# Optimization experiments

Hardware: AMD Instinct MI355X
Metric: run time of the kernel (lower is better)

## Reference

```python
import jax, jax.numpy as jnp
import numpy as np

D = 1024      # query_dim
H = 16        # heads
DH = 64       # dim_head
I = H * DH    # inner_dim = 1024
DC = 768      # context_dim
FF = 4 * D    # ff inner dim = 4096
EPS = 1e-5
SCALE = DH ** -0.5


def setup_inputs() -> dict:
    key = jax.random.key(0)
    ks = jax.random.split(key, 20)
    s = 0.02
    inp = {
        'x': jax.random.normal(ks[0], (2, 2048, D), jnp.float32),
        'context': jax.random.normal(ks[1], (2, 77, DC), jnp.float32),
        'ln1_g': jnp.ones((D,), jnp.float32), 'ln1_b': jnp.zeros((D,), jnp.float32),
        'ln2_g': jnp.ones((D,), jnp.float32), 'ln2_b': jnp.zeros((D,), jnp.float32),
        'ln3_g': jnp.ones((D,), jnp.float32), 'ln3_b': jnp.zeros((D,), jnp.float32),
        'Wq1': jax.random.normal(ks[2], (D, I), jnp.float32) * s,
        'Wk1': jax.random.normal(ks[3], (D, I), jnp.float32) * s,
        'Wv1': jax.random.normal(ks[4], (D, I), jnp.float32) * s,
        'Wo1': jax.random.normal(ks[5], (I, D), jnp.float32) * s,
        'bo1': jnp.zeros((D,), jnp.float32),
        'Wq2': jax.random.normal(ks[6], (D, I), jnp.float32) * s,
        'Wk2': jax.random.normal(ks[7], (DC, I), jnp.float32) * s,
        'Wv2': jax.random.normal(ks[8], (DC, I), jnp.float32) * s,
        'Wo2': jax.random.normal(ks[9], (I, D), jnp.float32) * s,
        'bo2': jnp.zeros((D,), jnp.float32),
        'Wff1': jax.random.normal(ks[10], (D, 2 * FF), jnp.float32) * s,
        'bff1': jnp.zeros((2 * FF,), jnp.float32),
        'Wff2': jax.random.normal(ks[11], (FF, D), jnp.float32) * s,
        'bff2': jnp.zeros((D,), jnp.float32),
    }
    return inp


def layer_norm(x, g, b):
    m = jnp.mean(x, axis=-1, keepdims=True)
    v = jnp.mean(jnp.square(x - m), axis=-1, keepdims=True)
    return (x - m) * jax.lax.rsqrt(v + EPS) * g + b


def cross_attention(x, ctx, Wq, Wk, Wv, Wo, bo):
    # x: [B,N,D], ctx: [B,M,Dc]
    B, N, _ = x.shape
    M = ctx.shape[1]
    q = (x @ Wq).reshape(B, N, H, DH).transpose(0, 2, 1, 3)    # [B,H,N,DH]
    k = (ctx @ Wk).reshape(B, M, H, DH).transpose(0, 2, 1, 3)  # [B,H,M,DH]
    v = (ctx @ Wv).reshape(B, M, H, DH).transpose(0, 2, 1, 3)
    sim = jnp.einsum('bhid,bhjd->bhij', q, k) * SCALE           # [B,H,N,M]
    attn = jax.nn.softmax(sim, axis=-1)
    out = jnp.einsum('bhij,bhjd->bhid', attn, v)                # [B,H,N,DH]
    out = out.transpose(0, 2, 1, 3).reshape(B, N, I)
    return out @ Wo + bo


def reference(x, context, ln1_g, ln1_b, ln2_g, ln2_b, ln3_g, ln3_b,
              Wq1, Wk1, Wv1, Wo1, bo1, Wq2, Wk2, Wv2, Wo2, bo2,
              Wff1, bff1, Wff2, bff2):
    # self-attention
    x = cross_attention(layer_norm(x, ln1_g, ln1_b), layer_norm(x, ln1_g, ln1_b),
                        Wq1, Wk1, Wv1, Wo1, bo1) + x
    # cross-attention
    x = cross_attention(layer_norm(x, ln2_g, ln2_b), context,
                        Wq2, Wk2, Wv2, Wo2, bo2) + x
    # GEGLU feed-forward
    hg = layer_norm(x, ln3_g, ln3_b) @ Wff1 + bff1
    h, gate = hg[..., :FF], hg[..., FF:]
    ff = (h * jax.nn.gelu(gate, approximate=False)) @ Wff2 + bff2
    return ff + x
```

## Files before the change

### kernel.cpp

```cpp
#include <hip/hip_runtime.h>
#include <hip/hip_bf16.h>
#include <math.h>

typedef short short8 __attribute__((ext_vector_type(8)));
typedef float floatx4 __attribute__((ext_vector_type(4)));
typedef unsigned short u16;

#define D_MODEL 1024
#define NH 16
#define DH 64
#define FF_DIM 4096

__device__ __forceinline__ u16 f2b(float f) {
  union { float f; unsigned u; } v; v.f = f;
  unsigned r = (v.u + 0x7fffu + ((v.u >> 16) & 1u)) >> 16;
  return (u16)r;
}
__device__ __forceinline__ u16 f2b_fast(float f) {
  union { float f; unsigned u; } v; v.f = f;
  return (u16)((v.u + 0x8000u) >> 16);
}
__device__ __forceinline__ float b2f(u16 h) {
  union { unsigned u; float f; } v; v.u = ((unsigned)h) << 16;
  return v.f;
}

__device__ __forceinline__ void gl_lds16(const u16* g, u16* l) {
  __builtin_amdgcn_global_load_lds(
      (const __attribute__((address_space(1))) unsigned int*)g,
      (__attribute__((address_space(3))) unsigned int*)l, 16, 0, 0);
}

__launch_bounds__(256)
__global__ void transpose_to_bf16(const float* __restrict__ in, u16* __restrict__ out,
                                  int K, int N, float scale) {
  __shared__ float tile[32][33];
  const int n0 = blockIdx.x * 32;
  const int k0 = blockIdx.y * 32;
  const int tx = threadIdx.x & 31;
  const int ty = threadIdx.x >> 5;
#pragma unroll
  for (int i = 0; i < 4; i++) {
    int k = k0 + ty + i * 8;
    tile[ty + i * 8][tx] = in[(size_t)k * N + (n0 + tx)] * scale;
  }
  __syncthreads();
#pragma unroll
  for (int i = 0; i < 4; i++) {
    int n = n0 + ty + i * 8;
    out[(size_t)n * K + (k0 + tx)] = f2b(tile[tx][ty + i * 8]);
  }
}

struct TransArgs {
  const float* src[6];
  u16* dst[6];
  float scale[6];
};

__launch_bounds__(256)
__global__ void transpose_to_bf16_multi(TransArgs a, int K, int N) {
  __shared__ float tile[32][33];
  const int z = blockIdx.z;
  const float* __restrict__ in = a.src[z];
  u16* __restrict__ out = a.dst[z];
  const float scale = a.scale[z];
  const int n0 = blockIdx.x * 32;
  const int k0 = blockIdx.y * 32;
  const int tx = threadIdx.x & 31;
  const int ty = threadIdx.x >> 5;
#pragma unroll
  for (int i = 0; i < 4; i++) {
    int k = k0 + ty + i * 8;
    tile[ty + i * 8][tx] = in[(size_t)k * N + (n0 + tx)] * scale;
  }
  __syncthreads();
#pragma unroll
  for (int i = 0; i < 4; i++) {
    int n = n0 + ty + i * 8;
    out[(size_t)n * K + (k0 + tx)] = f2b(tile[tx][ty + i * 8]);
  }
}

__launch_bounds__(256)
__global__ void convert_bf16(const float* __restrict__ in, u16* __restrict__ out, int n) {
  int i = blockIdx.x * 256 + threadIdx.x;
  if (i < n) out[i] = f2b(in[i]);
}

__launch_bounds__(256)
__global__ void ln_to_bf16(const float* __restrict__ x, const float* __restrict__ g,
                           const float* __restrict__ b, u16* __restrict__ out) {
  const int row = blockIdx.x;
  const int tid = threadIdx.x;
  const float4 v = ((const float4*)(x + (size_t)row * D_MODEL))[tid];
  float s = v.x + v.y + v.z + v.w;
  float ss = v.x * v.x + v.y * v.y + v.z * v.z + v.w * v.w;
#pragma unroll
  for (int o = 32; o; o >>= 1) { s += __shfl_xor(s, o); ss += __shfl_xor(ss, o); }
  __shared__ float red[8];
  const int wave = tid >> 6, lane = tid & 63;
  if (lane == 0) { red[wave] = s; red[4 + wave] = ss; }
  __syncthreads();
  const float st = red[0] + red[1] + red[2] + red[3];
  const float sst = red[4] + red[5] + red[6] + red[7];
  const float mean = st * (1.0f / D_MODEL);
  const float var = sst * (1.0f / D_MODEL) - mean * mean;
  const float rs = rsqrtf(var + 1e-5f);
  const float4 gv = ((const float4*)g)[tid];
  const float4 bv = ((const float4*)b)[tid];
  ushort4 o4;
  o4.x = f2b((v.x - mean) * rs * gv.x + bv.x);
  o4.y = f2b((v.y - mean) * rs * gv.y + bv.y);
  o4.z = f2b((v.z - mean) * rs * gv.z + bv.z);
  o4.w = f2b((v.w - mean) * rs * gv.w + bv.w);
  ((ushort4*)(out + (size_t)row * D_MODEL))[tid] = o4;
}

template <int EPI>
__launch_bounds__(256)
__global__ void gemm128(const u16* __restrict__ A, const u16* __restrict__ BT,
                        const float* __restrict__ bias, const float* __restrict__ resid,
                        float* __restrict__ Cf, u16* __restrict__ Cb, u16* __restrict__ VT,
                        int K, int lda, int ldb, int ldc) {
  __shared__ __attribute__((aligned(16))) u16 Al[128 * 64];
  __shared__ __attribute__((aligned(16))) u16 Bl[128 * 64];
  const int tid = threadIdx.x, wave = tid >> 6, lane = tid & 63;
  const int lm = lane & 15, lq = lane >> 4;
  const int wr = (wave >> 1) * 64, wc = (wave & 1) * 64;
  const int m0 = blockIdx.y * 128, n0 = blockIdx.x * 128;
  const int x8 = lm & 7;

  floatx4 acc[4][4] = {};

  for (int k0 = 0; k0 < K; k0 += 64) {
#pragma unroll
    for (int it = 0; it < 4; it++) {
      const int c = wave * 256 + it * 64 + lane;
      const int r = c >> 3, s = c & 7;
      const int lc = s ^ (r & 7);
      gl_lds16(A + (size_t)(m0 + r) * lda + k0 + lc * 8, &Al[c * 8]);
      gl_lds16(BT + (size_t)(n0 + r) * ldb + k0 + lc * 8, &Bl[c * 8]);
    }
    __syncthreads();
#pragma unroll
    for (int ks = 0; ks < 2; ks++) {
      short8 af[4], bf[4];
#pragma unroll
      for (int r = 0; r < 4; r++)
        af[r] = *(const short8*)(&Al[(wr + r * 16 + lm) * 64 + ((ks * 4 + lq) ^ x8) * 8]);
#pragma unroll
      for (int c = 0; c < 4; c++)
        bf[c] = *(const short8*)(&Bl[(wc + c * 16 + lm) * 64 + ((ks * 4 + lq) ^ x8) * 8]);
#pragma unroll
      for (int r = 0; r < 4; r++)
#pragma unroll
        for (int c = 0; c < 4; c++)
          acc[r][c] = __builtin_amdgcn_mfma_f32_16x16x32_bf16(af[r], bf[c], acc[r][c], 0, 0, 0);
    }
    __syncthreads();
  }

#pragma unroll
  for (int r = 0; r < 4; r++)
#pragma unroll
    for (int c = 0; c < 4; c++) {
      const int col = n0 + wc + c * 16 + lm;
      const int row0 = m0 + wr + r * 16 + lq * 4;
      if (EPI == 0) {
#pragma unroll
        for (int i = 0; i < 4; i++)
          Cb[(size_t)(row0 + i) * ldc + col] = f2b(acc[r][c][i]);
      } else if (EPI == 1) {
#pragma unroll
        for (int i = 0; i < 4; i++)
          Cf[(size_t)(row0 + i) * ldc + col] =
              acc[r][c][i] + bias[col] + resid[(size_t)(row0 + i) * ldc + col];
      } else {
        if (col < 2048) {
#pragma unroll
          for (int i = 0; i < 4; i++)
            Cb[(size_t)(row0 + i) * ldc + col] = f2b(acc[r][c][i]);
        } else {
          const int d = col - 2048;
          ushort4 pk;
          pk.x = f2b(acc[r][c][0]); pk.y = f2b(acc[r][c][1]);
          pk.z = f2b(acc[r][c][2]); pk.w = f2b(acc[r][c][3]);
          *(ushort4*)(&VT[((size_t)((row0 >> 11) * 1024 + d)) * 2048 + (row0 & 2047)]) = pk;
        }
      }
    }
}

template <int EPI>
__launch_bounds__(256)
__global__ void gemm_n64(const u16* __restrict__ A, const u16* __restrict__ BT,
                         const float* __restrict__ bias, const float* __restrict__ resid,
                         float* __restrict__ Cf, u16* __restrict__ Cb,
                         int K, int lda, int ldb, int ldc) {
  __shared__ __attribute__((aligned(16))) u16 Al[128 * 64];
  __shared__ __attribute__((aligned(16))) u16 Bl[64 * 64];
  const int tid = threadIdx.x, wave = tid >> 6, lane = tid & 63;
  const int lm = lane & 15, lq = lane >> 4;
  const int wr = (wave >> 1) * 64, wc = (wave & 1) * 32;
  const int m0 = blockIdx.y * 128, n0 = blockIdx.x * 64;
  const int x8 = lm & 7;

  floatx4 acc[4][2] = {};

  for (int k0 = 0; k0 < K; k0 += 64) {
#pragma unroll
    for (int it = 0; it < 4; it++) {
      const int c = wave * 256 + it * 64 + lane;
      const int r = c >> 3, s = c & 7;
      const int lc = s ^ (r & 7);
      gl_lds16(A + (size_t)(m0 + r) * lda + k0 + lc * 8, &Al[c * 8]);
    }
#pragma unroll
    for (int it = 0; it < 2; it++) {
      const int c = wave * 128 + it * 64 + lane;
      const int r = c >> 3, s = c & 7;
      const int lc = s ^ (r & 7);
      gl_lds16(BT + (size_t)(n0 + r) * ldb + k0 + lc * 8, &Bl[c * 8]);
    }
    __syncthreads();
#pragma unroll
    for (int ks = 0; ks < 2; ks++) {
      short8 af[4], bf[2];
#pragma unroll
      for (int r = 0; r < 4; r++)
        af[r] = *(const short8*)(&Al[(wr + r * 16 + lm) * 64 + ((ks * 4 + lq) ^ x8) * 8]);
#pragma unroll
      for (int c = 0; c < 2; c++)
        bf[c] = *(const short8*)(&Bl[(wc + c * 16 + lm) * 64 + ((ks * 4 + lq) ^ x8) * 8]);
#pragma unroll
      for (int r = 0; r < 4; r++)
#pragma unroll
        for (int c = 0; c < 2; c++)
          acc[r][c] = __builtin_amdgcn_mfma_f32_16x16x32_bf16(af[r], bf[c], acc[r][c], 0, 0, 0);
    }
    __syncthreads();
  }

#pragma unroll
  for (int r = 0; r < 4; r++)
#pragma unroll
    for (int c = 0; c < 2; c++) {
      const int col = n0 + wc + c * 16 + lm;
      const int row0 = m0 + wr + r * 16 + lq * 4;
      if (EPI == 0) {
#pragma unroll
        for (int i = 0; i < 4; i++)
          Cb[(size_t)(row0 + i) * ldc + col] = f2b(acc[r][c][i]);
      } else {
#pragma unroll
        for (int i = 0; i < 4; i++)
          Cf[(size_t)(row0 + i) * ldc + col] =
              acc[r][c][i] + bias[col] + resid[(size_t)(row0 + i) * ldc + col];
      }
    }
}

__launch_bounds__(256)
__global__ void gemm_geglu(const u16* __restrict__ A, const u16* __restrict__ BT,
                           const float* __restrict__ bias, u16* __restrict__ Cb,
                           int K, int lda, int ldb) {
  __shared__ __attribute__((aligned(16))) u16 Al[128 * 64];
  __shared__ __attribute__((aligned(16))) u16 Bl[64 * 64];
  __shared__ __attribute__((aligned(16))) u16 Bg[64 * 64];
  const int tid = threadIdx.x, wave = tid >> 6, lane = tid & 63;
  const int lm = lane & 15, lq = lane >> 4;
  const int wr = (wave >> 1) * 64, wc = (wave & 1) * 32;
  const int m0 = blockIdx.y * 128, n0 = blockIdx.x * 64;
  const int x8 = lm & 7;

  floatx4 acc[4][2] = {};
  floatx4 accg[4][2] = {};

  for (int k0 = 0; k0 < K; k0 += 64) {
#pragma unroll
    for (int it = 0; it < 4; it++) {
      const int c = wave * 256 + it * 64 + lane;
      const int r = c >> 3, s = c & 7;
      const int lc = s ^ (r & 7);
      gl_lds16(A + (size_t)(m0 + r) * lda + k0 + lc * 8, &Al[c * 8]);
    }
#pragma unroll
    for (int it = 0; it < 2; it++) {
      const int c = wave * 128 + it * 64 + lane;
      const int r = c >> 3, s = c & 7;
      const int lc = s ^ (r & 7);
      gl_lds16(BT + (size_t)(n0 + r) * ldb + k0 + lc * 8, &Bl[c * 8]);
      gl_lds16(BT + (size_t)(n0 + r + FF_DIM) * ldb + k0 + lc * 8, &Bg[c * 8]);
    }
    __syncthreads();
#pragma unroll
    for (int ks = 0; ks < 2; ks++) {
      short8 af[4], bf[2], bg[2];
#pragma unroll
      for (int r = 0; r < 4; r++)
        af[r] = *(const short8*)(&Al[(wr + r * 16 + lm) * 64 + ((ks * 4 + lq) ^ x8) * 8]);
#pragma unroll
      for (int c = 0; c < 2; c++) {
        bf[c] = *(const short8*)(&Bl[(wc + c * 16 + lm) * 64 + ((ks * 4 + lq) ^ x8) * 8]);
        bg[c] = *(const short8*)(&Bg[(wc + c * 16 + lm) * 64 + ((ks * 4 + lq) ^ x8) * 8]);
      }
#pragma unroll
      for (int r = 0; r < 4; r++)
#pragma unroll
        for (int c = 0; c < 2; c++) {
          acc[r][c] = __builtin_amdgcn_mfma_f32_16x16x32_bf16(af[r], bf[c], acc[r][c], 0, 0, 0);
          accg[r][c] = __builtin_amdgcn_mfma_f32_16x16x32_bf16(af[r], bg[c], accg[r][c], 0, 0, 0);
        }
    }
    __syncthreads();
  }

#pragma unroll
  for (int r = 0; r < 4; r++)
#pragma unroll
    for (int c = 0; c < 2; c++) {
      const int col = n0 + wc + c * 16 + lm;
#pragma unroll
      for (int i = 0; i < 4; i++) {
        const int row = m0 + wr + r * 16 + lq * 4 + i;
        const float h = acc[r][c][i] + bias[col];
        const float gt = accg[r][c][i] + bias[col + FF_DIM];
        const float gl = 0.5f * gt * (1.0f + erff(gt * 0.70710678118f));
        Cb[(size_t)row * FF_DIM + col] = f2b(h * gl);
      }
    }
}

#define BM 64
#define BN 64
#define LSTR 40

template <int TRANS>
__launch_bounds__(256)
__global__ void gemm_bt64(const u16* __restrict__ A, const u16* __restrict__ BT,
                          u16* __restrict__ Cb,
                          int M, int N, int K, int lda, int ldb, int ldc, int rowsPerB) {
  __shared__ __attribute__((aligned(16))) u16 Al[BM * LSTR];
  __shared__ __attribute__((aligned(16))) u16 Bl[BN * LSTR];
  const int tid = threadIdx.x, wave = tid >> 6, lane = tid & 63;
  const int wm = (wave >> 1) * 32, wn = (wave & 1) * 32;
  const int lm = lane & 15, lq = lane >> 4;
  const int m0 = blockIdx.y * BM, n0 = blockIdx.x * BN;

  floatx4 acc[2][2] = {};
  const int srow = tid >> 2;
  const int scol = (tid & 3) * 8;
  const bool a_ok = (m0 + srow) < M;

  for (int k0 = 0; k0 < K; k0 += 32) {
    int4 av = make_int4(0, 0, 0, 0);
    if (a_ok) av = *(const int4*)(A + (size_t)(m0 + srow) * lda + k0 + scol);
    *(int4*)(&Al[srow * LSTR + scol]) = av;
    int4 bv = *(const int4*)(BT + (size_t)(n0 + srow) * ldb + k0 + scol);
    *(int4*)(&Bl[srow * LSTR + scol]) = bv;
    __syncthreads();
    short8 af[2], bfr[2];
#pragma unroll
    for (int r = 0; r < 2; r++) af[r] = *(const short8*)(&Al[(wm + r * 16 + lm) * LSTR + lq * 8]);
#pragma unroll
    for (int c = 0; c < 2; c++) bfr[c] = *(const short8*)(&Bl[(wn + c * 16 + lm) * LSTR + lq * 8]);
#pragma unroll
    for (int r = 0; r < 2; r++)
#pragma unroll
      for (int c = 0; c < 2; c++)
        acc[r][c] = __builtin_amdgcn_mfma_f32_16x16x32_bf16(af[r], bfr[c], acc[r][c], 0, 0, 0);
    __syncthreads();
  }

#pragma unroll
  for (int r = 0; r < 2; r++)
#pragma unroll
    for (int c = 0; c < 2; c++) {
      const int col = n0 + wn + c * 16 + lm;
#pragma unroll
      for (int i = 0; i < 4; i++) {
        const int row = m0 + wm + r * 16 + lq * 4 + i;
        if (row < M) {
          if (TRANS == 0) {
            Cb[(size_t)row * ldc + col] = f2b(acc[r][c][i]);
          } else {
            const int bb = row / rowsPerB;
            const int n = row - bb * rowsPerB;
            Cb[((size_t)(bb * 1024 + col)) * 128 + n] = f2b(acc[r][c][i]);
          }
        }
      }
    }
}

__launch_bounds__(512)
__global__ void attn_mfma(const u16* __restrict__ Qg, const u16* __restrict__ Kg,
                          const u16* __restrict__ VTg, u16* __restrict__ Ob,
                          int N, int Mk, int kRowsPerBatch, int ldq, int ldk, int vtld) {
  const int ntiles = N / 128;
  const int bh = blockIdx.x / ntiles;
  const int qt = blockIdx.x % ntiles;
  const int b = bh / NH, h = bh % NH;
  const int tid = threadIdx.x, wave = tid >> 6, lane = tid & 63;
  const int lm = lane & 15, lq = lane >> 4;

  __shared__ __attribute__((aligned(16))) u16 Qs[128 * 64];
  __shared__ __attribute__((aligned(16))) u16 Ks[64 * 64];
  __shared__ __attribute__((aligned(16))) u16 Vt[64 * 64];
  __shared__ __attribute__((aligned(16))) u16 Ps[8][16 * 72];

  const u16* Qh = Qg + (size_t)b * N * ldq + h * DH;
  const u16* Kh = Kg + (size_t)b * kRowsPerBatch * ldk + h * DH;
  const u16* Vh = VTg + (size_t)(b * 1024 + h * DH) * vtld;

  {
    const u16* qsrc = Qh + (size_t)qt * 128 * ldq;
#pragma unroll
    for (int it = 0; it < 2; it++) {
      const int c = wave * 128 + it * 64 + lane;
      const int r = c >> 3, p = c & 7, lc = p ^ (r & 7);
      gl_lds16(qsrc + (size_t)r * ldq + lc * 8, &Qs[c * 8]);
    }
  }
  __syncthreads();
  short8 qf[2];
  qf[0] = *(const short8*)(&Qs[(wave * 16 + lm) * 64 + ((lq) ^ (lm & 7)) * 8]);
  qf[1] = *(const short8*)(&Qs[(wave * 16 + lm) * 64 + ((4 + lq) ^ (lm & 7)) * 8]);

  float lpart[4] = {0.f, 0.f, 0.f, 0.f};
  floatx4 o[4] = {};

  for (int kt = 0; kt < Mk; kt += 64) {
    __syncthreads();
    {
      const u16* ksrc = Kh + (size_t)kt * ldk;
      const u16* vsrc = Vh + kt;
      const int c = wave * 64 + lane;
      const int r = c >> 3, p = c & 7, lc = p ^ (r & 7);
      gl_lds16(ksrc + (size_t)r * ldk + lc * 8, &Ks[c * 8]);
      gl_lds16(vsrc + (size_t)r * vtld + lc * 8, &Vt[c * 8]);
    }
    __syncthreads();

    floatx4 s[4];
#pragma unroll
    for (int ct = 0; ct < 4; ct++) {
      short8 kf0 = *(const short8*)(&Ks[(ct * 16 + lm) * 64 + ((lq) ^ (lm & 7)) * 8]);
      short8 kf1 = *(const short8*)(&Ks[(ct * 16 + lm) * 64 + ((4 + lq) ^ (lm & 7)) * 8]);
      floatx4 z = {};
      z = __builtin_amdgcn_mfma_f32_16x16x32_bf16(qf[0], kf0, z, 0, 0, 0);
      z = __builtin_amdgcn_mfma_f32_16x16x32_bf16(qf[1], kf1, z, 0, 0, 0);
      s[ct] = z;
    }

    if (kt + 64 <= Mk) {
#pragma unroll
      for (int reg = 0; reg < 4; reg++) {
        float p0 = __expf(s[0][reg] - 16.0f);
        float p1 = __expf(s[1][reg] - 16.0f);
        float p2 = __expf(s[2][reg] - 16.0f);
        float p3 = __expf(s[3][reg] - 16.0f);
        lpart[reg] += (p0 + p1) + (p2 + p3);
        const int prow = (lq * 4 + reg) * 72;
        Ps[wave][prow + lm] = f2b_fast(p0);
        Ps[wave][prow + 16 + lm] = f2b_fast(p1);
        Ps[wave][prow + 32 + lm] = f2b_fast(p2);
        Ps[wave][prow + 48 + lm] = f2b_fast(p3);
      }
    } else {
#pragma unroll
      for (int reg = 0; reg < 4; reg++) {
        const int prow = (lq * 4 + reg) * 72;
        float psum = 0.f;
#pragma unroll
        for (int ct = 0; ct < 4; ct++) {
          const bool valid = (kt + ct * 16 + lm) < Mk;
          float p = valid ? __expf(s[ct][reg] - 16.0f) : 0.f;
          psum += p;
          Ps[wave][prow + ct * 16 + lm] = f2b_fast(p);
        }
        lpart[reg] += psum;
      }
    }

    const short8 pf0 = *(const short8*)(&Ps[wave][lm * 72 + lq * 8]);
    const short8 pf1 = *(const short8*)(&Ps[wave][lm * 72 + 32 + lq * 8]);
#pragma unroll
    for (int ct = 0; ct < 4; ct++) {
      short8 vf0 = *(const short8*)(&Vt[(ct * 16 + lm) * 64 + ((lq) ^ (lm & 7)) * 8]);
      short8 vf1 = *(const short8*)(&Vt[(ct * 16 + lm) * 64 + ((4 + lq) ^ (lm & 7)) * 8]);
      o[ct] = __builtin_amdgcn_mfma_f32_16x16x32_bf16(pf0, vf0, o[ct], 0, 0, 0);
      o[ct] = __builtin_amdgcn_mfma_f32_16x16x32_bf16(pf1, vf1, o[ct], 0, 0, 0);
    }
  }

  float inv[4];
#pragma unroll
  for (int reg = 0; reg < 4; reg++) {
    float l = lpart[reg];
    l += __shfl_xor(l, 1); l += __shfl_xor(l, 2);
    l += __shfl_xor(l, 4); l += __shfl_xor(l, 8);
    inv[reg] = 1.0f / l;
  }
#pragma unroll
  for (int ct = 0; ct < 4; ct++)
#pragma unroll
    for (int reg = 0; reg < 4; reg++) {
      const int grow = qt * 128 + wave * 16 + lq * 4 + reg;
      Ob[((size_t)(b * N + grow)) * D_MODEL + h * DH + ct * 16 + lm] =
          f2b(o[ct][reg] * inv[reg]);
    }
}

extern "C" void kernel_launch(void* const* d_in, const int* in_sizes, int n_in,
                              void* d_out, int out_size, void* d_ws, size_t ws_size,
                              hipStream_t stream) {
  const float* x    = (const float*)d_in[0];
  const float* ctx  = (const float*)d_in[1];
  const float* ln1g = (const float*)d_in[2];
  const float* ln1b = (const float*)d_in[3];
  const float* ln2g = (const float*)d_in[4];
  const float* ln2b = (const float*)d_in[5];
  const float* ln3g = (const float*)d_in[6];
  const float* ln3b = (const float*)d_in[7];
  const float* Wq1  = (const float*)d_in[8];
  const float* Wk1  = (const float*)d_in[9];
  const float* Wv1  = (const float*)d_in[10];
  const float* Wo1  = (const float*)d_in[11];
  const float* bo1  = (const float*)d_in[12];
  const float* Wq2  = (const float*)d_in[13];
  const float* Wk2  = (const float*)d_in[14];
  const float* Wv2  = (const float*)d_in[15];
  const float* Wo2  = (const float*)d_in[16];
  const float* bo2  = (const float*)d_in[17];
  const float* Wff1 = (const float*)d_in[18];
  const float* bff1 = (const float*)d_in[19];
  const float* Wff2 = (const float*)d_in[20];
  const float* bff2 = (const float*)d_in[21];
  float* out = (float*)d_out;

  char* ws = (char*)d_ws;
  size_t off = 0;
  auto alloc = [&](size_t bytes) -> char* {
    char* p = ws + off;
    off += (bytes + 255) & ~(size_t)255;
    return p;
  };
  u16* wqkv1T = (u16*)alloc((size_t)3072 * 1024 * 2);
  u16* wo1T   = (u16*)alloc((size_t)1024 * 1024 * 2);
  u16* wq2T   = (u16*)alloc((size_t)1024 * 1024 * 2);
  u16* wk2T   = (u16*)alloc((size_t)1024 * 768 * 2);
  u16* wv2T   = (u16*)alloc((size_t)1024 * 768 * 2);
  u16* wo2T   = (u16*)alloc((size_t)1024 * 1024 * 2);
  u16* wff1T  = (u16*)alloc((size_t)8192 * 1024 * 2);
  u16* wff2T  = (u16*)alloc((size_t)1024 * 4096 * 2);
  u16* xln    = (u16*)alloc((size_t)4096 * 1024 * 2);
  u16* ctxb   = (u16*)alloc((size_t)154 * 768 * 2);
  u16* QKVb   = (u16*)alloc((size_t)4096 * 3072 * 2);
  u16* VTb    = (u16*)alloc((size_t)2048 * 2048 * 2);
  u16* K2b    = (u16*)alloc((size_t)256 * 1024 * 2);
  u16* VT2b   = (u16*)alloc((size_t)2048 * 128 * 2);
  u16* Ob     = (u16*)alloc((size_t)4096 * 1024 * 2);
  float* x1   = (float*)alloc((size_t)4096 * 1024 * 4);
  float* x2   = (float*)alloc((size_t)4096 * 1024 * 4);
  u16* ffin   = (u16*)alloc((size_t)4096 * 4096 * 2);
  u16* Q2b    = ffin;

  dim3 blk(256);
  dim3 blk512(512);

  {
    TransArgs t6;
    t6.src[0] = Wq1;  t6.dst[0] = wqkv1T;                          t6.scale[0] = 1.0f;
    t6.src[1] = Wk1;  t6.dst[1] = wqkv1T + (size_t)1024 * 1024;    t6.scale[1] = 0.125f;
    t6.src[2] = Wv1;  t6.dst[2] = wqkv1T + (size_t)2048 * 1024;    t6.scale[2] = 1.0f;
    t6.src[3] = Wo1;  t6.dst[3] = wo1T;                            t6.scale[3] = 1.0f;
    t6.src[4] = Wq2;  t6.dst[4] = wq2T;                            t6.scale[4] = 1.0f;
    t6.src[5] = Wo2;  t6.dst[5] = wo2T;                            t6.scale[5] = 1.0f;
    transpose_to_bf16_multi<<<dim3(32, 32, 6), blk, 0, stream>>>(t6, 1024, 1024);
  }
  {
    TransArgs t2;
    t2.src[0] = Wk2;  t2.dst[0] = wk2T;  t2.scale[0] = 0.125f;
    t2.src[1] = Wv2;  t2.dst[1] = wv2T;  t2.scale[1] = 1.0f;
    t2.src[2] = Wk2;  t2.dst[2] = wk2T;  t2.scale[2] = 0.125f;
    t2.src[3] = Wk2;  t2.dst[3] = wk2T;  t2.scale[3] = 0.125f;
    t2.src[4] = Wk2;  t2.dst[4] = wk2T;  t2.scale[4] = 0.125f;
    t2.src[5] = Wk2;  t2.dst[5] = wk2T;  t2.scale[5] = 0.125f;
    transpose_to_bf16_multi<<<dim3(32, 24, 2), blk, 0, stream>>>(t2, 768, 1024);
  }
  transpose_to_bf16<<<dim3(256, 32), blk, 0, stream>>>(Wff1, wff1T, 1024, 8192, 1.0f);
  transpose_to_bf16<<<dim3(32, 128), blk, 0, stream>>>(Wff2, wff2T, 4096, 1024, 1.0f);
  convert_bf16<<<(154 * 768 + 255) / 256, blk, 0, stream>>>(ctx, ctxb, 154 * 768);

  ln_to_bf16<<<4096, blk, 0, stream>>>(x, ln1g, ln1b, xln);
  gemm128<2><<<dim3(24, 32), blk, 0, stream>>>(xln, wqkv1T, nullptr, nullptr, nullptr, QKVb,
                                               VTb, 1024, 1024, 1024, 3072);
  attn_mfma<<<2 * NH * (2048 / 128), blk512, 0, stream>>>(QKVb, QKVb + 1024, VTb, Ob,
                                                          2048, 2048, 2048, 3072, 3072, 2048);
  gemm_n64<1><<<dim3(16, 32), blk, 0, stream>>>(Ob, wo1T, bo1, x, x1, nullptr,
                                                1024, 1024, 1024, 1024);

  ln_to_bf16<<<4096, blk, 0, stream>>>(x1, ln2g, ln2b, xln);
  gemm_n64<0><<<dim3(16, 32), blk, 0, stream>>>(xln, wq2T, nullptr, nullptr, nullptr, Q2b,
                                                1024, 1024, 1024, 1024);
  gemm_bt64<0><<<dim3(16, 3), blk, 0, stream>>>(ctxb, wk2T, K2b, 154, 1024, 768, 768, 768, 1024, 77);
  gemm_bt64<1><<<dim3(16, 3), blk, 0, stream>>>(ctxb, wv2T, VT2b, 154, 1024, 768, 768, 768, 1024, 77);
  attn_mfma<<<2 * NH * (2048 / 128), blk512, 0, stream>>>(Q2b, K2b, VT2b, Ob,
                                                          2048, 77, 77, 1024, 1024, 128);
  gemm_n64<1><<<dim3(16, 32), blk, 0, stream>>>(Ob, wo2T, bo2, x1, x2, nullptr,
                                                1024, 1024, 1024, 1024);

  ln_to_bf16<<<4096, blk, 0, stream>>>(x2, ln3g, ln3b, xln);
  gemm_geglu<<<dim3(64, 32), blk, 0, stream>>>(xln, wff1T, bff1, ffin, 1024, 1024, 1024);
  gemm_n64<1><<<dim3(16, 32), blk, 0, stream>>>(ffin, wff2T, bff2, x2, out, nullptr,
                                                4096, 4096, 4096, 1024);
}
```

Measured before the change: 511.1 us.

## Merge weight transposes into one launch and double-buffer GEGLU GEMM

All ten weight transpose-to-bf16 conversions now run in a single kernel launch that uses a flat block index and a per-tensor start table, replacing four separate launches. The GEGLU GEMM gains double-buffered LDS staging, so the next K-tile's global-to-LDS loads are issued before computing on the current tile, hiding load latency. LDS use doubles to roughly 64KB per block, which may lower occupancy. The per-block tensor lookup adds a few scalar instructions per block.

```diff
diff --git a/kernel.cpp b/kernel.cpp
--- a/kernel.cpp
+++ b/kernel.cpp
@@ -31,42 +31,31 @@
       (__attribute__((address_space(3))) unsigned int*)l, 16, 0, 0);
 }
 
+struct PrepArgs {
+  const float* src[10];
+  u16* dst[10];
+  float scale[10];
+  int start[10];
+  int bx[10];
+  int K[10];
+  int N[10];
+};
+
 __launch_bounds__(256)
-__global__ void transpose_to_bf16(const float* __restrict__ in, u16* __restrict__ out,
-                                  int K, int N, float scale) {
+__global__ void transpose_multi10(PrepArgs a) {
   __shared__ float tile[32][33];
-  const int n0 = blockIdx.x * 32;
-  const int k0 = blockIdx.y * 32;
-  const int tx = threadIdx.x & 31;
-  const int ty = threadIdx.x >> 5;
-#pragma unroll
-  for (int i = 0; i < 4; i++) {
-    int k = k0 + ty + i * 8;
-    tile[ty + i * 8][tx] = in[(size_t)k * N + (n0 + tx)] * scale;
-  }
-  __syncthreads();
-#pragma unroll
-  for (int i = 0; i < 4; i++) {
-    int n = n0 + ty + i * 8;
-    out[(size_t)n * K + (k0 + tx)] = f2b(tile[tx][ty + i * 8]);
-  }
-}
-
-struct TransArgs {
-  const float* src[6];
-  u16* dst[6];
-  float scale[6];
-};
-
-__launch_bounds__(256)
-__global__ void transpose_to_bf16_multi(TransArgs a, int K, int N) {
-  __shared__ float tile[32][33];
-  const int z = blockIdx.z;
+  const int bid = blockIdx.x;
+  int z = 0;
+#pragma unroll
+  for (int i = 1; i < 10; i++)
+    if (bid >= a.start[i]) z = i;
   const float* __restrict__ in = a.src[z];
   u16* __restrict__ out = a.dst[z];
   const float scale = a.scale[z];
-  const int n0 = blockIdx.x * 32;
-  const int k0 = blockIdx.y * 32;
+  const int K = a.K[z], N = a.N[z];
+  const int local = bid - a.start[z];
+  const int n0 = (local % a.bx[z]) * 32;
+  const int k0 = (local / a.bx[z]) * 32;
   const int tx = threadIdx.x & 31;
   const int ty = threadIdx.x >> 5;
 #pragma unroll
@@ -265,9 +254,9 @@
 __global__ void gemm_geglu(const u16* __restrict__ A, const u16* __restrict__ BT,
                            const float* __restrict__ bias, u16* __restrict__ Cb,
                            int K, int lda, int ldb) {
-  __shared__ __attribute__((aligned(16))) u16 Al[128 * 64];
-  __shared__ __attribute__((aligned(16))) u16 Bl[64 * 64];
-  __shared__ __attribute__((aligned(16))) u16 Bg[64 * 64];
+  __shared__ __attribute__((aligned(16))) u16 Al[2][128 * 64];
+  __shared__ __attribute__((aligned(16))) u16 Bl[2][64 * 64];
+  __shared__ __attribute__((aligned(16))) u16 Bg[2][64 * 64];
   const int tid = threadIdx.x, wave = tid >> 6, lane = tid & 63;
   const int lm = lane & 15, lq = lane >> 4;
   const int wr = (wave >> 1) * 64, wc = (wave & 1) * 32;
@@ -277,33 +266,41 @@
   floatx4 acc[4][2] = {};
   floatx4 accg[4][2] = {};
 
-  for (int k0 = 0; k0 < K; k0 += 64) {
+  auto stage = [&](int k0, int buf) {
 #pragma unroll
     for (int it = 0; it < 4; it++) {
       const int c = wave * 256 + it * 64 + lane;
       const int r = c >> 3, s = c & 7;
       const int lc = s ^ (r & 7);
-      gl_lds16(A + (size_t)(m0 + r) * lda + k0 + lc * 8, &Al[c * 8]);
+      gl_lds16(A + (size_t)(m0 + r) * lda + k0 + lc * 8, &Al[buf][c * 8]);
     }
 #pragma unroll
     for (int it = 0; it < 2; it++) {
       const int c = wave * 128 + it * 64 + lane;
       const int r = c >> 3, s = c & 7;
       const int lc = s ^ (r & 7);
-      gl_lds16(BT + (size_t)(n0 + r) * ldb + k0 + lc * 8, &Bl[c * 8]);
-      gl_lds16(BT + (size_t)(n0 + r + FF_DIM) * ldb + k0 + lc * 8, &Bg[c * 8]);
-    }
-    __syncthreads();
+      gl_lds16(BT + (size_t)(n0 + r) * ldb + k0 + lc * 8, &Bl[buf][c * 8]);
+      gl_lds16(BT + (size_t)(n0 + r + FF_DIM) * ldb + k0 + lc * 8, &Bg[buf][c * 8]);
+    }
+  };
+
+  stage(0, 0);
+  __syncthreads();
+
+  const int nt = K >> 6;
+  int cur = 0;
+  for (int t = 0; t < nt; ++t) {
+    if (t + 1 < nt) stage((t + 1) << 6, cur ^ 1);
 #pragma unroll
     for (int ks = 0; ks < 2; ks++) {
       short8 af[4], bf[2], bg[2];
 #pragma unroll
       for (int r = 0; r < 4; r++)
-        af[r] = *(const short8*)(&Al[(wr + r * 16 + lm) * 64 + ((ks * 4 + lq) ^ x8) * 8]);
+        af[r] = *(const short8*)(&Al[cur][(wr + r * 16 + lm) * 64 + ((ks * 4 + lq) ^ x8) * 8]);
 #pragma unroll
       for (int c = 0; c < 2; c++) {
-        bf[c] = *(const short8*)(&Bl[(wc + c * 16 + lm) * 64 + ((ks * 4 + lq) ^ x8) * 8]);
-        bg[c] = *(const short8*)(&Bg[(wc + c * 16 + lm) * 64 + ((ks * 4 + lq) ^ x8) * 8]);
+        bf[c] = *(const short8*)(&Bl[cur][(wc + c * 16 + lm) * 64 + ((ks * 4 + lq) ^ x8) * 8]);
+        bg[c] = *(const short8*)(&Bg[cur][(wc + c * 16 + lm) * 64 + ((ks * 4 + lq) ^ x8) * 8]);
       }
 #pragma unroll
       for (int r = 0; r < 4; r++)
@@ -314,6 +311,7 @@
         }
     }
     __syncthreads();
+    cur ^= 1;
   }
 
 #pragma unroll
@@ -571,27 +569,24 @@
   dim3 blk512(512);
 
   {
-    TransArgs t6;
-    t6.src[0] = Wq1;  t6.dst[0] = wqkv1T;                          t6.scale[0] = 1.0f;
-    t6.src[1] = Wk1;  t6.dst[1] = wqkv1T + (size_t)1024 * 1024;    t6.scale[1] = 0.125f;
-    t6.src[2] = Wv1;  t6.dst[2] = wqkv1T + (size_t)2048 * 1024;    t6.scale[2] = 1.0f;
-    t6.src[3] = Wo1;  t6.dst[3] = wo1T;                            t6.scale[3] = 1.0f;
-    t6.src[4] = Wq2;  t6.dst[4] = wq2T;                            t6.scale[4] = 1.0f;
-    t6.src[5] = Wo2;  t6.dst[5] = wo2T;                            t6.scale[5] = 1.0f;
-    transpose_to_bf16_multi<<<dim3(32, 32, 6), blk, 0, stream>>>(t6, 1024, 1024);
-  }
-  {
-    TransArgs t2;
-    t2.src[0] = Wk2;  t2.dst[0] = wk2T;  t2.scale[0] = 0.125f;
-    t2.src[1] = Wv2;  t2.dst[1] = wv2T;  t2.scale[1] = 1.0f;
-    t2.src[2] = Wk2;  t2.dst[2] = wk2T;  t2.scale[2] = 0.125f;
-    t2.src[3] = Wk2;  t2.dst[3] = wk2T;  t2.scale[3] = 0.125f;
-    t2.src[4] = Wk2;  t2.dst[4] = wk2T;  t2.scale[4] = 0.125f;
-    t2.src[5] = Wk2;  t2.dst[5] = wk2T;  t2.scale[5] = 0.125f;
-    transpose_to_bf16_multi<<<dim3(32, 24, 2), blk, 0, stream>>>(t2, 768, 1024);
-  }
-  transpose_to_bf16<<<dim3(256, 32), blk, 0, stream>>>(Wff1, wff1T, 1024, 8192, 1.0f);
-  transpose_to_bf16<<<dim3(32, 128), blk, 0, stream>>>(Wff2, wff2T, 4096, 1024, 1.0f);
+    PrepArgs p;
+    p.src[0] = Wq1;  p.dst[0] = wqkv1T;                        p.scale[0] = 1.0f;
+    p.src[1] = Wk1;  p.dst[1] = wqkv1T + (size_t)1024 * 1024;  p.scale[1] = 0.125f;
+    p.src[2] = Wv1;  p.dst[2] = wqkv1T + (size_t)2048 * 1024;  p.scale[2] = 1.0f;
+    p.src[3] = Wo1;  p.dst[3] = wo1T;                          p.scale[3] = 1.0f;
+    p.src[4] = Wq2;  p.dst[4] = wq2T;                          p.scale[4] = 1.0f;
+    p.src[5] = Wo2;  p.dst[5] = wo2T;                          p.scale[5] = 1.0f;
+    p.src[6] = Wk2;  p.dst[6] = wk2T;                          p.scale[6] = 0.125f;
+    p.src[7] = Wv2;  p.dst[7] = wv2T;                          p.scale[7] = 1.0f;
+    p.src[8] = Wff1; p.dst[8] = wff1T;                         p.scale[8] = 1.0f;
+    p.src[9] = Wff2; p.dst[9] = wff2T;                         p.scale[9] = 1.0f;
+    int st = 0;
+    for (int i = 0; i < 6; i++) { p.start[i] = st; p.bx[i] = 32; p.K[i] = 1024; p.N[i] = 1024; st += 1024; }
+    for (int i = 6; i < 8; i++) { p.start[i] = st; p.bx[i] = 32; p.K[i] = 768;  p.N[i] = 1024; st += 768; }
+    p.start[8] = st; p.bx[8] = 256; p.K[8] = 1024; p.N[8] = 8192; st += 8192;
+    p.start[9] = st; p.bx[9] = 32;  p.K[9] = 4096; p.N[9] = 1024; st += 4096;
+    transpose_multi10<<<dim3(st), blk, 0, stream>>>(p);
+  }
   convert_bf16<<<(154 * 768 + 255) / 256, blk, 0, stream>>>(ctx, ctxb, 154 * 768);
 
   ln_to_bf16<<<4096, blk, 0, stream>>>(x, ln1g, ln1b, xln);
```

New measurement: 514.4 us. No clear change (+0.6%).
